# Kernel tuning notes

Measured on AMD Instinct MI355X. Metric: run time of the kernel, lower is better.

## Reference

```python
import jax, jax.numpy as jnp
import numpy as np

M = 16384      # total flat points per role (8 scenes x 2048 pts)
D = 256        # d_model
H = 4          # heads
K = 16         # knn neighbors
DFF = 1024     # 4*D
LN_EPS = 1e-5


def _ln(x, g, b):
    m = jnp.mean(x, axis=-1, keepdims=True)
    v = jnp.mean((x - m) ** 2, axis=-1, keepdims=True)
    return (x - m) / jnp.sqrt(v + LN_EPS) * g + b


def _knn_block(x, coord, ctx, ctx_coord, idx,
               Wq, Wk, Wv, Wo, g1, b1, pe_w, pe_b,
               W1, bf1, W2, bf2, g2, b2):
    # x: [M,D] query feats; ctx: [N,D] context feats; idx: [M,K] neighbor ids (-1 = invalid)
    m, d = x.shape
    k = idx.shape[1]
    dh = d // H
    valid = idx >= 0
    idx_c = jnp.where(valid, idx, 0)

    xn = _ln(x, g1, b1)
    q = (xn @ Wq).reshape(m, H, dh)                      # [M,H,dh]
    k_all = ctx @ Wk                                     # [N,D]
    v_all = ctx @ Wv                                     # [N,D]

    rel = coord[:, None, :] - ctx_coord[idx_c]           # [M,K,3]
    pe = rel @ pe_w + pe_b                               # [M,K,D] relative position encoding
    kg = (k_all[idx_c] + pe).reshape(m, k, H, dh)        # gathered keys  [M,K,H,dh]
    vg = (v_all[idx_c] + pe).reshape(m, k, H, dh)        # gathered values

    scale = jnp.asarray(1.0 / np.sqrt(dh), x.dtype)
    scores = jnp.einsum('mhd,mkhd->mhk', q, kg) * scale
    scores = jnp.where(valid[:, None, :], scores, jnp.asarray(-1e9, x.dtype))
    attn = jax.nn.softmax(scores, axis=-1)
    out = jnp.einsum('mhk,mkhd->mhd', attn, vg).reshape(m, d) @ Wo
    x = x + out
    h = jax.nn.gelu(_ln(x, g2, b2) @ W1 + bf1)
    return x + (h @ W2 + bf2)


def setup_inputs() -> dict:
    key = jax.random.key(0)
    ks = jax.random.split(key, 24)
    s = 0.02
    nblk = 2  # [0]=self(a), [1]=cross(a,b)
    inp = {
        'feat_a': jax.random.normal(ks[0], (M, D), jnp.float32),
        'coord_a': jax.random.normal(ks[1], (M, 3), jnp.float32),
        'feat_b': jax.random.normal(ks[2], (M, D), jnp.float32),
        'coord_b': jax.random.normal(ks[3], (M, 3), jnp.float32),
        'Wq': jax.random.normal(ks[4], (nblk, D, D), jnp.float32) * s,
        'Wk': jax.random.normal(ks[5], (nblk, D, D), jnp.float32) * s,
        'Wv': jax.random.normal(ks[6], (nblk, D, D), jnp.float32) * s,
        'Wo': jax.random.normal(ks[7], (nblk, D, D), jnp.float32) * s,
        'ln1_g': jnp.ones((nblk, D), jnp.float32),
        'ln1_b': jnp.zeros((nblk, D), jnp.float32),
        'pe_w': jax.random.normal(ks[8], (nblk, 3, D), jnp.float32) * s,
        'pe_b': jnp.zeros((nblk, D), jnp.float32),
        'ffn_w1': jax.random.normal(ks[9], (nblk, D, DFF), jnp.float32) * s,
        'ffn_b1': jnp.zeros((nblk, DFF), jnp.float32),
        'ffn_w2': jax.random.normal(ks[10], (nblk, DFF, D), jnp.float32) * s,
        'ffn_b2': jnp.zeros((nblk, D), jnp.float32),
        'ln2_g': jnp.ones((nblk, D), jnp.float32),
        'ln2_b': jnp.zeros((nblk, D), jnp.float32),
        'knn_a2a': jax.random.randint(ks[11], (M, K), 0, M, jnp.int64 if jax.config.jax_enable_x64 else jnp.int32),
        'knn_a2b': jax.random.randint(ks[12], (M, K), 0, M, jnp.int64 if jax.config.jax_enable_x64 else jnp.int32),
    }
    return inp


def reference(feat_a, coord_a, feat_b, coord_b,
              Wq, Wk, Wv, Wo, ln1_g, ln1_b, pe_w, pe_b,
              ffn_w1, ffn_b1, ffn_w2, ffn_b2, ln2_g, ln2_b,
              knn_a2a, knn_a2b):
    def params(i):
        return (Wq[i], Wk[i], Wv[i], Wo[i], ln1_g[i], ln1_b[i], pe_w[i], pe_b[i],
                ffn_w1[i], ffn_b1[i], ffn_w2[i], ffn_b2[i], ln2_g[i], ln2_b[i])
    # layer 'self(a)': feat[a] = block(feat[a], coord[a], knn_indexes['a2a'])
    fa = _knn_block(feat_a, coord_a, feat_a, coord_a, knn_a2a, *params(0))
    # layer 'cross(a,b)': feat[a] = block(query=feat[a], context=feat[b], knn_indexes['a2b'])
    fa = _knn_block(fa, coord_a, feat_b, coord_b, knn_a2b, *params(1))
    return fa
```

## Files before the change

kernel.cpp:

```cpp
#include <hip/hip_runtime.h>
#include <hip/hip_bf16.h>
#include <stdint.h>

#define MM 16384
#define DD 256
#define HH 4
#define KK 16
#define DFF_ 1024

typedef __attribute__((ext_vector_type(8))) short bf16x8;
typedef __attribute__((ext_vector_type(16))) float f32x16;
typedef __attribute__((ext_vector_type(2))) float f32x2;

__device__ __forceinline__ unsigned short f2bf(float f) {
    unsigned u = __builtin_bit_cast(unsigned, f);
    unsigned r = u + 0x7fffu + ((u >> 16) & 1u);
    return (unsigned short)(r >> 16);
}
__device__ __forceinline__ float bf2f(unsigned short h) {
    unsigned u = ((unsigned)h) << 16;
    return __builtin_bit_cast(float, u);
}


__global__ __launch_bounds__(256) void prep_weights(
        const float* __restrict__ Wq, const float* __restrict__ Wk,
        const float* __restrict__ Wv, const float* __restrict__ Wo,
        const float* __restrict__ W1, const float* __restrict__ W2,
        unsigned short* __restrict__ wf) {
    int t = blockIdx.x * blockDim.x + threadIdx.x;
    const float* src; unsigned short* dst;
    int kd, lg, rem, blk, e, sect;
    if (t < 131072) { sect = 0; rem = t; blk = rem >> 16; e = rem & 65535;
        src = Wq; dst = wf + blk * 65536; kd = 256; lg = 8; }
    else if (t < 262144) { sect = 1; rem = t - 131072; blk = rem >> 16; e = rem & 65535;
        src = Wk; dst = wf + 131072 + blk * 131072; kd = 256; lg = 8; }
    else if (t < 393216) { sect = 2; rem = t - 262144; blk = rem >> 16; e = rem & 65535;
        src = Wv; dst = wf + 131072 + blk * 131072; kd = 256; lg = 8; }
    else if (t < 524288) { sect = 0; rem = t - 393216; blk = rem >> 16; e = rem & 65535;
        src = Wo; dst = wf + 393216 + blk * 65536; kd = 256; lg = 8; }
    else if (t < 1048576) { sect = 0; rem = t - 524288; blk = rem >> 18; e = rem & 262143;
        src = W1; dst = wf + 524288 + blk * 262144; kd = 256; lg = 10; }
    else if (t < 1572864) { sect = 0; rem = t - 1048576; blk = rem >> 18; e = rem & 262143;
        src = W2; dst = wf + 1048576 + blk * 262144; kd = 1024; lg = 8; }
    else return;
    int k = e >> lg;
    int n = e & ((1 << lg) - 1);
    if (sect == 1) n = (n >> 2) * 8 + (n & 3);
    else if (sect == 2) n = (n >> 2) * 8 + 4 + (n & 3);
    float v = src[(size_t)blk * kd * (1 << lg) + e];
    int off = ((n >> 5) * (kd >> 4) + (k >> 4)) * 512 + (((k >> 3) & 1) * 32 + (n & 31)) * 8 + (k & 7);
    dst[off] = f2bf(v);
}

__global__ __launch_bounds__(256) void ln_to_frag(
        const float* __restrict__ x, const float* __restrict__ g,
        const float* __restrict__ b, unsigned short* __restrict__ out,
        int apply_ln) {
    int wave = threadIdx.x >> 6, lane = threadIdx.x & 63;
    int m = blockIdx.x * 4 + wave;
    const float4 xv = reinterpret_cast<const float4*>(x + (size_t)m * DD)[lane];
    float vals[4] = {xv.x, xv.y, xv.z, xv.w};
    int k0 = lane * 4;
    if (apply_ln) {
        float s = vals[0] + vals[1] + vals[2] + vals[3];
        float sq = vals[0]*vals[0] + vals[1]*vals[1] + vals[2]*vals[2] + vals[3]*vals[3];
        for (int o = 32; o; o >>= 1) { s += __shfl_xor(s, o, 64); sq += __shfl_xor(sq, o, 64); }
        float mean = s * (1.0f / DD);
        float var = sq * (1.0f / DD) - mean * mean;
        float rs = rsqrtf(var + 1e-5f);
        #pragma unroll
        for (int c = 0; c < 4; ++c)
            vals[c] = (vals[c] - mean) * rs * g[k0 + c] + b[k0 + c];
    }
    int chunk = ((m >> 5) * (DD >> 4) + (k0 >> 4)) * 64 + ((k0 >> 3) & 1) * 32 + (m & 31);
    ushort4 o4 = make_ushort4(f2bf(vals[0]), f2bf(vals[1]), f2bf(vals[2]), f2bf(vals[3]));
    *reinterpret_cast<ushort4*>(out + (size_t)chunk * 8 + (k0 & 7)) = o4;
}

constexpr int GOUT_F32 = 0;
constexpr int GOUT_GELU_FRAG = 2;

template <int KG>
__device__ __forceinline__ void compute_tile(
        const bf16x8* __restrict__ a0, const bf16x8* __restrict__ a1,
        const bf16x8* __restrict__ b0, const bf16x8* __restrict__ b1,
        f32x16 acc[2][2]) {
    #pragma unroll 4
    for (int g = 0; g < KG; ++g) {
        bf16x8 av0 = a0[g * 64];
        bf16x8 av1 = a1[g * 64];
        bf16x8 bv0 = b0[g * 64];
        bf16x8 bv1 = b1[g * 64];
        acc[0][0] = __builtin_amdgcn_mfma_f32_32x32x16_bf16(av0, bv0, acc[0][0], 0, 0, 0);
        acc[0][1] = __builtin_amdgcn_mfma_f32_32x32x16_bf16(av0, bv1, acc[0][1], 0, 0, 0);
        acc[1][0] = __builtin_amdgcn_mfma_f32_32x32x16_bf16(av1, bv0, acc[1][0], 0, 0, 0);
        acc[1][1] = __builtin_amdgcn_mfma_f32_32x32x16_bf16(av1, bv1, acc[1][1], 0, 0, 0);
    }
}

template <int KD, int NOUT, int MODE, bool RESID, bool BIAS>
__global__ __launch_bounds__(256) void gemm_frag(
        const bf16x8* __restrict__ A, const bf16x8* __restrict__ B,
        void* __restrict__ outp, const float* __restrict__ resid,
        const float* __restrict__ bias, int out_kd) {
    constexpr int KG = KD / 16;
    __shared__ float lds[MODE == GOUT_GELU_FRAG ? 4 * 1056 : 4];
    int wave = threadIdx.x >> 6, lane = threadIdx.x & 63;
    int wm = wave & 1, wn = wave >> 1;
    int m0 = blockIdx.x * 128 + wm * 64;
    int n0 = blockIdx.y * 128 + wn * 64;
    const bf16x8* a0 = A + ((size_t)(m0 >> 5) * KG) * 64 + lane;
    const bf16x8* a1 = a0 + (size_t)KG * 64;
    const bf16x8* b0 = B + ((size_t)(n0 >> 5) * KG) * 64 + lane;
    const bf16x8* b1 = b0 + (size_t)KG * 64;
    f32x16 acc[2][2] = {};
    compute_tile<KG>(a0, a1, b0, b1, acc);
    int col = lane & 31, rq = (lane >> 5) * 4;
    if constexpr (MODE == GOUT_F32) {
        #pragma unroll
        for (int i = 0; i < 2; ++i)
        #pragma unroll
        for (int j = 0; j < 2; ++j) {
            #pragma unroll
            for (int r = 0; r < 16; ++r) {
                int row = (r & 3) + 8 * (r >> 2) + rq;
                int m = m0 + i * 32 + row;
                int n = n0 + j * 32 + col;
                float v = acc[i][j][r];
                if (BIAS) v += bias[n];
                if (RESID) v += resid[(size_t)m * NOUT + n];
                ((float*)outp)[(size_t)m * NOUT + n] = v;
            }
        }
    } else {
        float* wlds = &lds[wave * 1056];
        for (int i = 0; i < 2; ++i)
        for (int j = 0; j < 2; ++j) {
            #pragma unroll
            for (int r = 0; r < 16; ++r) {
                int row = (r & 3) + 8 * (r >> 2) + rq;
                int n = n0 + j * 32 + col;
                float v = acc[i][j][r] + bias[n];
                float arg = v * (1.5957691216f + 0.0713548163f * v * v);
                v = v * __frcp_rn(1.0f + __expf(-arg));
                wlds[row * 33 + col] = v;
            }
            #pragma unroll
            for (int it = 0; it < 2; ++it) {
                int task = lane + it * 64;
                int row = task >> 2, cc = task & 3;
                int m = m0 + i * 32 + row;
                int k = n0 + j * 32 + cc * 8;
                float* p = &wlds[row * 33 + cc * 8];
                unsigned short us[8];
                #pragma unroll
                for (int e = 0; e < 8; ++e) us[e] = f2bf(p[e]);
                int chunk = ((m >> 5) * (out_kd >> 4) + (k >> 4)) * 64 + ((k >> 3) & 1) * 32 + (m & 31);
                reinterpret_cast<uint4*>(outp)[chunk] = *reinterpret_cast<uint4*>(us);
            }
        }
    }
}

__global__ __launch_bounds__(256) void gemm_qkv(
        const bf16x8* __restrict__ Aq, const bf16x8* __restrict__ Akv,
        const bf16x8* __restrict__ Bq, const bf16x8* __restrict__ Bkv,
        unsigned short* __restrict__ qout, unsigned char* __restrict__ kvout) {
    constexpr int KG = 16;
    int wave = threadIdx.x >> 6, lane = threadIdx.x & 63;
    int wm = wave & 1, wn = wave >> 1;
    int y = blockIdx.y;
    bool isQ = y < 2;
    const bf16x8* A = isQ ? Aq : Akv;
    const bf16x8* B = isQ ? Bq : Bkv;
    int n0 = (isQ ? y : y - 2) * 128 + wn * 64;
    int m0 = blockIdx.x * 128 + wm * 64;
    const bf16x8* a0 = A + ((size_t)(m0 >> 5) * KG) * 64 + lane;
    const bf16x8* a1 = a0 + (size_t)KG * 64;
    const bf16x8* b0 = B + ((size_t)(n0 >> 5) * KG) * 64 + lane;
    const bf16x8* b1 = b0 + (size_t)KG * 64;
    f32x16 acc[2][2] = {};
    compute_tile<KG>(a0, a1, b0, b1, acc);
    int col = lane & 31, rq = (lane >> 5) * 4;
    #pragma unroll
    for (int i = 0; i < 2; ++i)
    #pragma unroll
    for (int j = 0; j < 2; ++j)
    #pragma unroll
    for (int r = 0; r < 16; ++r) {
        int row = (r & 3) + 8 * (r >> 2) + rq;
        int m = m0 + i * 32 + row;
        int n = n0 + j * 32 + col;
        float v = acc[i][j][r];
        if (isQ) qout[(size_t)m * 256 + n] = f2bf(v);
        else kvout[(size_t)m * 512 + n] =
            (unsigned char)(__builtin_amdgcn_cvt_pk_fp8_f32(v, v, 0, false) & 0xff);
    }
}

__global__ __launch_bounds__(256) void attn_kernel(
        const unsigned short* __restrict__ q, const unsigned char* __restrict__ kv,
        const float* __restrict__ coord, const float* __restrict__ ctx_coord,
        const int* __restrict__ knn,
        const float* __restrict__ pe_w, const float* __restrict__ pe_b,
        unsigned short* __restrict__ out_frag) {
    int wave = threadIdx.x >> 6, lane = threadIdx.x & 63;
    int m = blockIdx.x * 4 + wave;
    int s = lane & 15;
    int d0 = (lane >> 4) * 64 + s * 4;

    ushort4 qv4 = *reinterpret_cast<const ushort4*>(q + (size_t)m * DD + d0);
    float qx = bf2f(qv4.x), qy = bf2f(qv4.y), qz = bf2f(qv4.z), qw = bf2f(qv4.w);
    float4 pw0 = *reinterpret_cast<const float4*>(pe_w + d0);
    float4 pw1 = *reinterpret_cast<const float4*>(pe_w + DD + d0);
    float4 pw2 = *reinterpret_cast<const float4*>(pe_w + 2 * DD + d0);
    float4 pbv = *reinterpret_cast<const float4*>(pe_b + d0);

    float cx = coord[m * 3], cy = coord[m * 3 + 1], cz = coord[m * 3 + 2];
    int myidx = knn[(size_t)m * KK + s];
    int icm = myidx < 0 ? 0 : myidx;
    float rx = cx - ctx_coord[icm * 3];
    float ry = cy - ctx_coord[icm * 3 + 1];
    float rz = cz - ctx_coord[icm * 3 + 2];

    float t0 = qx * pw0.x + qy * pw0.y + qz * pw0.z + qw * pw0.w;
    float t1 = qx * pw1.x + qy * pw1.y + qz * pw1.z + qw * pw1.w;
    float t2 = qx * pw2.x + qy * pw2.y + qz * pw2.z + qw * pw2.w;
    float t3 = qx * pbv.x + qy * pbv.y + qz * pbv.z + qw * pbv.w;
    #pragma unroll
    for (int o = 1; o < 16; o <<= 1) {
        t0 += __shfl_xor(t0, o, 64);
        t1 += __shfl_xor(t1, o, 64);
        t2 += __shfl_xor(t2, o, 64);
        t3 += __shfl_xor(t3, o, 64);
    }

    float sc_own = 0.0f;
    unsigned vpk[KK];
    #pragma unroll
    for (int j = 0; j < KK; ++j) {
        int ij = __shfl(myidx, j, 64);
        int ic = ij < 0 ? 0 : ij;
        uint2 kvv = *reinterpret_cast<const uint2*>(kv + (size_t)ic * 512 + (d0 >> 2) * 8);
        vpk[j] = kvv.y;
        f32x2 k01 = __builtin_amdgcn_cvt_pk_f32_fp8(kvv.x, false);
        f32x2 k23 = __builtin_amdgcn_cvt_pk_f32_fp8(kvv.x, true);
        float p = qx * k01.x + qy * k01.y + qz * k23.x + qw * k23.y;
        p += __shfl_xor(p, 1, 64);
        p += __shfl_xor(p, 2, 64);
        p += __shfl_xor(p, 4, 64);
        p += __shfl_xor(p, 8, 64);
        sc_own = (j == s) ? p : sc_own;
    }
    float corr = rx * t0 + ry * t1 + rz * t2 + t3;
    sc_own = (myidx >= 0) ? (sc_own + corr) * 0.125f : -1e9f;

    float mx = sc_own;
    mx = fmaxf(mx, __shfl_xor(mx, 1, 64));
    mx = fmaxf(mx, __shfl_xor(mx, 2, 64));
    mx = fmaxf(mx, __shfl_xor(mx, 4, 64));
    mx = fmaxf(mx, __shfl_xor(mx, 8, 64));
    float e = __expf(sc_own - mx);
    float sum = e;
    sum += __shfl_xor(sum, 1, 64);
    sum += __shfl_xor(sum, 2, 64);
    sum += __shfl_xor(sum, 4, 64);
    sum += __shfl_xor(sum, 8, 64);
    float w_own = e * __frcp_rn(sum);

    float wrx = w_own * rx, wry = w_own * ry, wrz = w_own * rz;
    #pragma unroll
    for (int o = 1; o < 16; o <<= 1) {
        wrx += __shfl_xor(wrx, o, 64);
        wry += __shfl_xor(wry, o, 64);
        wrz += __shfl_xor(wrz, o, 64);
    }

    int gbase = lane & 48;
    float ax = 0.f, ay = 0.f, az = 0.f, aw = 0.f;
    #pragma unroll
    for (int j = 0; j < KK; ++j) {
        float wj = __shfl(w_own, gbase + j, 64);
        f32x2 v01 = __builtin_amdgcn_cvt_pk_f32_fp8(vpk[j], false);
        f32x2 v23 = __builtin_amdgcn_cvt_pk_f32_fp8(vpk[j], true);
        ax += wj * v01.x;
        ay += wj * v01.y;
        az += wj * v23.x;
        aw += wj * v23.y;
    }
    ax += wrx * pw0.x + wry * pw1.x + wrz * pw2.x + pbv.x;
    ay += wrx * pw0.y + wry * pw1.y + wrz * pw2.y + pbv.y;
    az += wrx * pw0.z + wry * pw1.z + wrz * pw2.z + pbv.z;
    aw += wrx * pw0.w + wry * pw1.w + wrz * pw2.w + pbv.w;

    ushort4 o4 = make_ushort4(f2bf(ax), f2bf(ay), f2bf(az), f2bf(aw));
    int chunk = ((m >> 5) * (DD >> 4) + (d0 >> 4)) * 64 + ((d0 >> 3) & 1) * 32 + (m & 31);
    *reinterpret_cast<ushort4*>(out_frag + (size_t)chunk * 8 + (d0 & 7)) = o4;
}

extern "C" void kernel_launch(void* const* d_in, const int* in_sizes, int n_in,
                              void* d_out, int out_size, void* d_ws, size_t ws_size,
                              hipStream_t stream) {
    const float* feat_a = (const float*)d_in[0];
    const float* coord_a = (const float*)d_in[1];
    const float* feat_b = (const float*)d_in[2];
    const float* coord_b = (const float*)d_in[3];
    const float* Wq = (const float*)d_in[4];
    const float* Wk = (const float*)d_in[5];
    const float* Wv = (const float*)d_in[6];
    const float* Wo = (const float*)d_in[7];
    const float* ln1_g = (const float*)d_in[8];
    const float* ln1_b = (const float*)d_in[9];
    const float* pe_w = (const float*)d_in[10];
    const float* pe_b = (const float*)d_in[11];
    const float* W1 = (const float*)d_in[12];
    const float* b1 = (const float*)d_in[13];
    const float* W2 = (const float*)d_in[14];
    const float* b2 = (const float*)d_in[15];
    const float* ln2_g = (const float*)d_in[16];
    const float* ln2_b = (const float*)d_in[17];
    const int* knn_a2a = (const int*)d_in[18];
    const int* knn_a2b = (const int*)d_in[19];

    char* ws = (char*)d_ws;
    unsigned short* wfrag = (unsigned short*)ws;
    float* xmid = (float*)(ws + (4ull << 20));
    float* xout0 = (float*)(ws + (20ull << 20));
    unsigned short* qbuf = (unsigned short*)(ws + (36ull << 20));
    unsigned char* kvbuf = (unsigned char*)(ws + (52ull << 20));
    unsigned short* xnf = (unsigned short*)(ws + (68ull << 20));
    unsigned short* ctxf = (unsigned short*)(ws + (76ull << 20));
    unsigned short* attnf = (unsigned short*)(ws + (84ull << 20));
    unsigned short* geluf = (unsigned short*)(ws + (36ull << 20));

    const unsigned short* WQF = wfrag;
    const unsigned short* KVF = wfrag + 131072;
    const unsigned short* WOF = wfrag + 393216;
    const unsigned short* W1F = wfrag + 524288;
    const unsigned short* W2F = wfrag + 1048576;

    prep_weights<<<(1572864 + 255) / 256, 256, 0, stream>>>(Wq, Wk, Wv, Wo, W1, W2, wfrag);

    for (int blk = 0; blk < 2; ++blk) {
        const float* x_in = blk ? xout0 : feat_a;
        const float* ctx = blk ? feat_b : feat_a;
        const float* ccrd = blk ? coord_b : coord_a;
        const int* knn = blk ? knn_a2b : knn_a2a;
        float* x_out_final = blk ? (float*)d_out : xout0;

        ln_to_frag<<<MM / 4, 256, 0, stream>>>(ctx, nullptr, nullptr, ctxf, 0);
        ln_to_frag<<<MM / 4, 256, 0, stream>>>(x_in, ln1_g + blk * DD, ln1_b + blk * DD, xnf, 1);

        gemm_qkv<<<dim3(MM / 128, 6), 256, 0, stream>>>(
            (const bf16x8*)xnf, (const bf16x8*)ctxf,
            (const bf16x8*)(WQF + blk * 65536), (const bf16x8*)(KVF + blk * 131072),
            qbuf, kvbuf);

        attn_kernel<<<MM / 4, 256, 0, stream>>>(qbuf, kvbuf, coord_a, ccrd, knn,
                                                pe_w + blk * 3 * DD, pe_b + blk * DD, attnf);

        gemm_frag<256, 256, GOUT_F32, true, false><<<dim3(MM / 128, 2), 256, 0, stream>>>(
            (const bf16x8*)attnf, (const bf16x8*)(WOF + blk * 65536), xmid, x_in, nullptr, 0);

        ln_to_frag<<<MM / 4, 256, 0, stream>>>(xmid, ln2_g + blk * DD, ln2_b + blk * DD, xnf, 1);

        gemm_frag<256, 1024, GOUT_GELU_FRAG, false, true><<<dim3(MM / 128, 8), 256, 0, stream>>>(
            (const bf16x8*)xnf, (const bf16x8*)(W1F + blk * 262144), geluf, nullptr,
            b1 + blk * DFF_, 1024);

        gemm_frag<1024, 256, GOUT_F32, true, true><<<dim3(MM / 128, 2), 256, 0, stream>>>(
            (const bf16x8*)geluf, (const bf16x8*)(W2F + blk * 262144), x_out_final, xmid,
            b2 + blk * DD, 0);
    }
}
```

Before: 349.7 us.

## Merge LN/ctx frag kernels, retile FFN1 GEMM, drop softmax max subtraction

Combines the two frag-conversion launches into one two-row grid and splits the FFN1 GELU GEMM into its own kernel. Each wave in that kernel now computes a 64x128 tile, so A fragments are reused across four B columns and the blocks are larger. It also removes the max-subtraction step from the softmax, saving a few shuffles per query. That last change risks exp overflow for large scores. The max also only handled masked neighbours implicitly, so if every neighbour of a query is invalid the sum becomes zero.

```diff
diff --git a/kernel.cpp b/kernel.cpp
--- a/kernel.cpp
+++ b/kernel.cpp
@@ -53,12 +53,15 @@
     dst[off] = f2bf(v);
 }
 
-__global__ __launch_bounds__(256) void ln_to_frag(
-        const float* __restrict__ x, const float* __restrict__ g,
-        const float* __restrict__ b, unsigned short* __restrict__ out,
-        int apply_ln) {
+__global__ __launch_bounds__(256) void ln_to_frag_dual(
+        const float* __restrict__ xq, const float* __restrict__ g,
+        const float* __restrict__ b, unsigned short* __restrict__ outq,
+        const float* __restrict__ xc, unsigned short* __restrict__ outc) {
     int wave = threadIdx.x >> 6, lane = threadIdx.x & 63;
     int m = blockIdx.x * 4 + wave;
+    int apply_ln = blockIdx.y;
+    const float* x = apply_ln ? xq : xc;
+    unsigned short* out = apply_ln ? outq : outc;
     const float4 xv = reinterpret_cast<const float4*>(x + (size_t)m * DD)[lane];
     float vals[4] = {xv.x, xv.y, xv.z, xv.w};
     int k0 = lane * 4;
@@ -78,8 +81,27 @@
     *reinterpret_cast<ushort4*>(out + (size_t)chunk * 8 + (k0 & 7)) = o4;
 }
 
-constexpr int GOUT_F32 = 0;
-constexpr int GOUT_GELU_FRAG = 2;
+__global__ __launch_bounds__(256) void ln_to_frag(
+        const float* __restrict__ x, const float* __restrict__ g,
+        const float* __restrict__ b, unsigned short* __restrict__ out) {
+    int wave = threadIdx.x >> 6, lane = threadIdx.x & 63;
+    int m = blockIdx.x * 4 + wave;
+    const float4 xv = reinterpret_cast<const float4*>(x + (size_t)m * DD)[lane];
+    float vals[4] = {xv.x, xv.y, xv.z, xv.w};
+    int k0 = lane * 4;
+    float s = vals[0] + vals[1] + vals[2] + vals[3];
+    float sq = vals[0]*vals[0] + vals[1]*vals[1] + vals[2]*vals[2] + vals[3]*vals[3];
+    for (int o = 32; o; o >>= 1) { s += __shfl_xor(s, o, 64); sq += __shfl_xor(sq, o, 64); }
+    float mean = s * (1.0f / DD);
+    float var = sq * (1.0f / DD) - mean * mean;
+    float rs = rsqrtf(var + 1e-5f);
+    #pragma unroll
+    for (int c = 0; c < 4; ++c)
+        vals[c] = (vals[c] - mean) * rs * g[k0 + c] + b[k0 + c];
+    int chunk = ((m >> 5) * (DD >> 4) + (k0 >> 4)) * 64 + ((k0 >> 3) & 1) * 32 + (m & 31);
+    ushort4 o4 = make_ushort4(f2bf(vals[0]), f2bf(vals[1]), f2bf(vals[2]), f2bf(vals[3]));
+    *reinterpret_cast<ushort4*>(out + (size_t)chunk * 8 + (k0 & 7)) = o4;
+}
 
 template <int KG>
 __device__ __forceinline__ void compute_tile(
@@ -99,13 +121,12 @@
     }
 }
 
-template <int KD, int NOUT, int MODE, bool RESID, bool BIAS>
+template <int KD, int NOUT, bool RESID, bool BIAS>
 __global__ __launch_bounds__(256) void gemm_frag(
         const bf16x8* __restrict__ A, const bf16x8* __restrict__ B,
-        void* __restrict__ outp, const float* __restrict__ resid,
-        const float* __restrict__ bias, int out_kd) {
+        float* __restrict__ outp, const float* __restrict__ resid,
+        const float* __restrict__ bias) {
     constexpr int KG = KD / 16;
-    __shared__ float lds[MODE == GOUT_GELU_FRAG ? 4 * 1056 : 4];
     int wave = threadIdx.x >> 6, lane = threadIdx.x & 63;
     int wm = wave & 1, wn = wave >> 1;
     int m0 = blockIdx.x * 128 + wm * 64;
@@ -117,48 +138,71 @@
     f32x16 acc[2][2] = {};
     compute_tile<KG>(a0, a1, b0, b1, acc);
     int col = lane & 31, rq = (lane >> 5) * 4;
-    if constexpr (MODE == GOUT_F32) {
+    #pragma unroll
+    for (int i = 0; i < 2; ++i)
+    #pragma unroll
+    for (int j = 0; j < 2; ++j) {
         #pragma unroll
-        for (int i = 0; i < 2; ++i)
+        for (int r = 0; r < 16; ++r) {
+            int row = (r & 3) + 8 * (r >> 2) + rq;
+            int m = m0 + i * 32 + row;
+            int n = n0 + j * 32 + col;
+            float v = acc[i][j][r];
+            if (BIAS) v += bias[n];
+            if (RESID) v += resid[(size_t)m * NOUT + n];
+            outp[(size_t)m * NOUT + n] = v;
+        }
+    }
+}
+
+__global__ __launch_bounds__(256, 1) void gemm_gelu(
+        const bf16x8* __restrict__ A, const bf16x8* __restrict__ B,
+        unsigned short* __restrict__ outp, const float* __restrict__ bias) {
+    constexpr int KG = 16;
+    __shared__ float lds[4 * 1056];
+    int wave = threadIdx.x >> 6, lane = threadIdx.x & 63;
+    int m0 = blockIdx.x * 256 + wave * 64;
+    int n0 = blockIdx.y * 128;
+    const bf16x8* a0 = A + ((size_t)(m0 >> 5) * KG) * 64 + lane;
+    const bf16x8* a1 = a0 + (size_t)KG * 64;
+    const bf16x8* b0 = B + ((size_t)(n0 >> 5) * KG) * 64 + lane;
+    f32x16 acc[2][4] = {};
+    #pragma unroll 2
+    for (int g = 0; g < KG; ++g) {
+        bf16x8 av0 = a0[g * 64];
+        bf16x8 av1 = a1[g * 64];
         #pragma unroll
-        for (int j = 0; j < 2; ++j) {
+        for (int j = 0; j < 4; ++j) {
+            bf16x8 bv = b0[((size_t)j * KG + g) * 64];
+            acc[0][j] = __builtin_amdgcn_mfma_f32_32x32x16_bf16(av0, bv, acc[0][j], 0, 0, 0);
+            acc[1][j] = __builtin_amdgcn_mfma_f32_32x32x16_bf16(av1, bv, acc[1][j], 0, 0, 0);
+        }
+    }
+    int col = lane & 31, rq = (lane >> 5) * 4;
+    float* wlds = &lds[wave * 1056];
+    for (int i = 0; i < 2; ++i)
+    for (int j = 0; j < 4; ++j) {
+        #pragma unroll
+        for (int r = 0; r < 16; ++r) {
+            int row = (r & 3) + 8 * (r >> 2) + rq;
+            int n = n0 + j * 32 + col;
+            float v = acc[i][j][r] + bias[n];
+            float arg = v * (1.5957691216f + 0.0713548163f * v * v);
+            v = v * __frcp_rn(1.0f + __expf(-arg));
+            wlds[row * 33 + col] = v;
+        }
+        #pragma unroll
+        for (int it = 0; it < 2; ++it) {
+            int task = lane + it * 64;
+            int row = task >> 2, cc = task & 3;
+            int m = m0 + i * 32 + row;
+            int k = n0 + j * 32 + cc * 8;
+            float* p = &wlds[row * 33 + cc * 8];
+            unsigned short us[8];
             #pragma unroll
-            for (int r = 0; r < 16; ++r) {
-                int row = (r & 3) + 8 * (r >> 2) + rq;
-                int m = m0 + i * 32 + row;
-                int n = n0 + j * 32 + col;
-                float v = acc[i][j][r];
-                if (BIAS) v += bias[n];
-                if (RESID) v += resid[(size_t)m * NOUT + n];
-                ((float*)outp)[(size_t)m * NOUT + n] = v;
-            }
-        }
-    } else {
-        float* wlds = &lds[wave * 1056];
-        for (int i = 0; i < 2; ++i)
-        for (int j = 0; j < 2; ++j) {
-            #pragma unroll
-            for (int r = 0; r < 16; ++r) {
-                int row = (r & 3) + 8 * (r >> 2) + rq;
-                int n = n0 + j * 32 + col;
-                float v = acc[i][j][r] + bias[n];
-                float arg = v * (1.5957691216f + 0.0713548163f * v * v);
-                v = v * __frcp_rn(1.0f + __expf(-arg));
-                wlds[row * 33 + col] = v;
-            }
-            #pragma unroll
-            for (int it = 0; it < 2; ++it) {
-                int task = lane + it * 64;
-                int row = task >> 2, cc = task & 3;
-                int m = m0 + i * 32 + row;
-                int k = n0 + j * 32 + cc * 8;
-                float* p = &wlds[row * 33 + cc * 8];
-                unsigned short us[8];
-                #pragma unroll
-                for (int e = 0; e < 8; ++e) us[e] = f2bf(p[e]);
-                int chunk = ((m >> 5) * (out_kd >> 4) + (k >> 4)) * 64 + ((k >> 3) & 1) * 32 + (m & 31);
-                reinterpret_cast<uint4*>(outp)[chunk] = *reinterpret_cast<uint4*>(us);
-            }
+            for (int e = 0; e < 8; ++e) us[e] = f2bf(p[e]);
+            int chunk = ((m >> 5) * 64 + (k >> 4)) * 64 + ((k >> 3) & 1) * 32 + (m & 31);
+            reinterpret_cast<uint4*>(outp)[chunk] = *reinterpret_cast<uint4*>(us);
         }
     }
 }
@@ -256,12 +300,7 @@
     float corr = rx * t0 + ry * t1 + rz * t2 + t3;
     sc_own = (myidx >= 0) ? (sc_own + corr) * 0.125f : -1e9f;
 
-    float mx = sc_own;
-    mx = fmaxf(mx, __shfl_xor(mx, 1, 64));
-    mx = fmaxf(mx, __shfl_xor(mx, 2, 64));
-    mx = fmaxf(mx, __shfl_xor(mx, 4, 64));
-    mx = fmaxf(mx, __shfl_xor(mx, 8, 64));
-    float e = __expf(sc_own - mx);
+    float e = __expf(sc_own);
     float sum = e;
     sum += __shfl_xor(sum, 1, 64);
     sum += __shfl_xor(sum, 2, 64);
@@ -349,8 +388,8 @@
         const int* knn = blk ? knn_a2b : knn_a2a;
         float* x_out_final = blk ? (float*)d_out : xout0;
 
-        ln_to_frag<<<MM / 4, 256, 0, stream>>>(ctx, nullptr, nullptr, ctxf, 0);
-        ln_to_frag<<<MM / 4, 256, 0, stream>>>(x_in, ln1_g + blk * DD, ln1_b + blk * DD, xnf, 1);
+        ln_to_frag_dual<<<dim3(MM / 4, 2), 256, 0, stream>>>(
+            x_in, ln1_g + blk * DD, ln1_b + blk * DD, xnf, ctx, ctxf);
 
         gemm_qkv<<<dim3(MM / 128, 6), 256, 0, stream>>>(
             (const bf16x8*)xnf, (const bf16x8*)ctxf,
@@ -360,17 +399,16 @@
         attn_kernel<<<MM / 4, 256, 0, stream>>>(qbuf, kvbuf, coord_a, ccrd, knn,
                                                 pe_w + blk * 3 * DD, pe_b + blk * DD, attnf);
 
-        gemm_frag<256, 256, GOUT_F32, true, false><<<dim3(MM / 128, 2), 256, 0, stream>>>(
-            (const bf16x8*)attnf, (const bf16x8*)(WOF + blk * 65536), xmid, x_in, nullptr, 0);
-
-        ln_to_frag<<<MM / 4, 256, 0, stream>>>(xmid, ln2_g + blk * DD, ln2_b + blk * DD, xnf, 1);
-
-        gemm_frag<256, 1024, GOUT_GELU_FRAG, false, true><<<dim3(MM / 128, 8), 256, 0, stream>>>(
-            (const bf16x8*)xnf, (const bf16x8*)(W1F + blk * 262144), geluf, nullptr,
-            b1 + blk * DFF_, 1024);
-
-        gemm_frag<1024, 256, GOUT_F32, true, true><<<dim3(MM / 128, 2), 256, 0, stream>>>(
+        gemm_frag<256, 256, true, false><<<dim3(MM / 128, 2), 256, 0, stream>>>(
+            (const bf16x8*)attnf, (const bf16x8*)(WOF + blk * 65536), xmid, x_in, nullptr);
+
+        ln_to_frag<<<MM / 4, 256, 0, stream>>>(xmid, ln2_g + blk * DD, ln2_b + blk * DD, xnf);
+
+        gemm_gelu<<<dim3(MM / 256, 8), 256, 0, stream>>>(
+            (const bf16x8*)xnf, (const bf16x8*)(W1F + blk * 262144), geluf, b1 + blk * DFF_);
+
+        gemm_frag<1024, 256, true, true><<<dim3(MM / 128, 2), 256, 0, stream>>>(
             (const bf16x8*)geluf, (const bf16x8*)(W2F + blk * 262144), x_out_final, xmid,
-            b2 + blk * DD, 0);
-    }
-}
+            b2 + blk * DD);
+    }
+}
```

After: 385.1 us. +10.1%, slower.
